# Kernel optimization log

Measured on AMD Instinct MI355X. Metric: run time of the kernel, lower is better.

The kernel has to match this reference:

```python
import jax, jax.numpy as jnp
import numpy as np

B, L, D, H, K = 2, 2048, 1024, 16, 32  # batch, seqlen, model dim, heads, max_rel_pos
DK = D // H


def setup_inputs() -> dict:
    key = jax.random.key(0)
    ks = jax.random.split(key, 12)
    inp = {
        "query": jax.random.normal(ks[0], (B, L, D), jnp.float32),
        "key": jax.random.normal(ks[1], (B, L, D), jnp.float32),
        "value": jax.random.normal(ks[2], (B, L, D), jnp.float32),
        "mask": jnp.ones((B, L, L), jnp.bool_),
        # Linear params (stored [in, out], applied x @ W + b)
        "Wq": jax.random.normal(ks[3], (D, D), jnp.float32) * 0.02,
        "bq": jnp.zeros((D,), jnp.float32),
        "Wk": jax.random.normal(ks[4], (D, D), jnp.float32) * 0.02,
        "bk": jnp.zeros((D,), jnp.float32),
        "Wv": jax.random.normal(ks[5], (D, D), jnp.float32) * 0.02,
        "bv": jnp.zeros((D,), jnp.float32),
        "Wo": jax.random.normal(ks[6], (D, D), jnp.float32) * 0.02,
        "bo": jnp.zeros((D,), jnp.float32),
        "rel_emb": jax.random.normal(ks[7], (2 * K + 1, DK), jnp.float32) * 0.02,
    }
    return inp


def _rel_pos_matrix(length, max_rel):
    r = jnp.arange(length)
    dist = r[None, :] - r[:, None]  # [i,j] = j - i
    return jnp.clip(dist, -max_rel, max_rel) + max_rel  # in [0, 2K]


def reference(query, key, value, mask, Wq, bq, Wk, bk, Wv, bv, Wo, bo, rel_emb):
    b, l, d = query.shape
    dk = d // H
    shape = lambda x: x.reshape(b, l, H, dk).transpose(0, 2, 1, 3)  # -> [b,h,l,dk]

    q = shape(query @ Wq + bq) / jnp.sqrt(jnp.asarray(dk, query.dtype))
    k = shape(key @ Wk + bk)
    v = shape(value @ Wv + bv)

    relpos = rel_emb[_rel_pos_matrix(l, K)]  # [l, l, dk]

    # scores: content + relative-key term
    scores = jnp.einsum("bhid,bhjd->bhij", q, k) + jnp.einsum("bhid,ijd->bhij", q, relpos)
    scores = jnp.where(mask[:, None, :, :], scores, -1e18)
    attn = jax.nn.softmax(scores, axis=-1)  # dropout is identity in eval

    # context: content + relative-value term
    ctx = jnp.einsum("bhij,bhjd->bhid", attn, v) + jnp.einsum("bhij,ijd->bhid", attn, relpos)
    x = ctx.transpose(0, 2, 1, 3).reshape(b, l, d)
    return x @ Wo + bo
```

## Files before the change

kernel.cpp:

```cpp
#include <hip/hip_runtime.h>
#include <hip/hip_bf16.h>
#include <stdint.h>

#define B_  2
#define L_  2048
#define D_  1024
#define H_  16
#define DK_ 64
#define M0L 6.0f
#define QSCALE 0.18033688011112042f
#define KVS 80

using bf16x8 = __attribute__((ext_vector_type(8))) short;
using f32x4  = __attribute__((ext_vector_type(4))) float;

static __device__ __forceinline__ unsigned short f2bf(float f) {
  unsigned int u = __builtin_bit_cast(unsigned int, f);
  u += 0x7FFFu + ((u >> 16) & 1u);
  return (unsigned short)(u >> 16);
}
static __device__ __forceinline__ float bf2f(unsigned short h) {
  unsigned int u = ((unsigned int)h) << 16;
  return __builtin_bit_cast(float, u);
}
static __device__ __forceinline__ unsigned packbf(float lo, float hi) {
  __hip_bfloat162 h2 = __float22bfloat162_rn(make_float2(lo, hi));
  unsigned r;
  __builtin_memcpy(&r, &h2, 4);
  return r;
}
static __device__ __forceinline__ bf16x8 mkfrag(unsigned a, unsigned b, unsigned c, unsigned d) {
  union { unsigned u[4]; bf16x8 v; } x;
  x.u[0] = a; x.u[1] = b; x.u[2] = c; x.u[3] = d;
  return x.v;
}
static __device__ __forceinline__ float aexp2(float x) {
  float r;
  asm("v_exp_f32 %0, %1" : "=v"(r) : "v"(x));
  return r;
}

__global__ __launch_bounds__(256) void k_prep(const float* __restrict__ q,
                                              const float* __restrict__ k,
                                              const float* __restrict__ v,
                                              unsigned short* __restrict__ xq,
                                              unsigned short* __restrict__ xk,
                                              unsigned short* __restrict__ xv,
                                              const float* __restrict__ W0,
                                              const float* __restrict__ W1,
                                              const float* __restrict__ W2,
                                              const float* __restrict__ W3,
                                              unsigned short* __restrict__ T0,
                                              unsigned short* __restrict__ T1,
                                              unsigned short* __restrict__ T2,
                                              unsigned short* __restrict__ T3) {
  __shared__ float ts[64][65];
  const int bx = blockIdx.x;
  const int tid = threadIdx.x;
  if (bx < 6144) {
    const int z = bx >> 11;
    const float* src = (z == 0) ? q : (z == 1) ? k : v;
    unsigned short* dst = (z == 0) ? xq : (z == 1) ? xk : xv;
    int i = (bx & 2047) * 256 + tid;
    float4 a = *(const float4*)(src + (size_t)i * 8);
    float4 b = *(const float4*)(src + (size_t)i * 8 + 4);
    union { unsigned short u[8]; uint4 v4; } o;
    o.u[0] = f2bf(a.x); o.u[1] = f2bf(a.y); o.u[2] = f2bf(a.z); o.u[3] = f2bf(a.w);
    o.u[4] = f2bf(b.x); o.u[5] = f2bf(b.y); o.u[6] = f2bf(b.z); o.u[7] = f2bf(b.w);
    *(uint4*)(dst + (size_t)i * 8) = o.v4;
  } else {
    const int r = bx - 6144;
    const int z = r >> 8, rem = r & 255;
    const float* W = (z == 0) ? W0 : (z == 1) ? W1 : (z == 2) ? W2 : W3;
    unsigned short* Wt = (z == 0) ? T0 : (z == 1) ? T1 : (z == 2) ? T2 : T3;
    const int n0 = (rem & 15) * 64, k0 = (rem >> 4) * 64;
#pragma unroll
    for (int it = 0; it < 4; ++it) {
      int idx = tid + it * 256;
      int row = idx >> 4, c4 = idx & 15;
      float4 vv = *(const float4*)&W[(size_t)(k0 + row) * 1024 + n0 + c4 * 4];
      ts[row][c4 * 4 + 0] = vv.x; ts[row][c4 * 4 + 1] = vv.y;
      ts[row][c4 * 4 + 2] = vv.z; ts[row][c4 * 4 + 3] = vv.w;
    }
    __syncthreads();
#pragma unroll
    for (int it = 0; it < 4; ++it) {
      int idx = tid + it * 256;
      int n = idx >> 4, c4 = idx & 15;
      ushort4 o;
      o.x = f2bf(ts[c4 * 4 + 0][n]); o.y = f2bf(ts[c4 * 4 + 1][n]);
      o.z = f2bf(ts[c4 * 4 + 2][n]); o.w = f2bf(ts[c4 * 4 + 3][n]);
      *(ushort4*)&Wt[(size_t)(n0 + n) * 1024 + k0 + c4 * 4] = o;
    }
  }
}

__global__ __launch_bounds__(256) void k_gemm_qkv(const unsigned short* __restrict__ XQ,
                                                  const unsigned short* __restrict__ XK,
                                                  const unsigned short* __restrict__ XV,
                                                  const unsigned short* __restrict__ WQ,
                                                  const unsigned short* __restrict__ WK,
                                                  const unsigned short* __restrict__ WV,
                                                  const float* __restrict__ bqp,
                                                  const float* __restrict__ bkp,
                                                  const float* __restrict__ bvp,
                                                  unsigned short* __restrict__ QBH,
                                                  unsigned short* __restrict__ KBH,
                                                  unsigned short* __restrict__ VT) {
  __shared__ __align__(16) unsigned short As[128 * 32];
  __shared__ __align__(16) unsigned short Bs[128 * 32];
  const int bid = blockIdx.x;
  const int xcd = bid & 7, nn = (bid >> 3) & 7, gq = bid >> 6;
  const int grp = gq * 8 + xcd;
  const int sel = grp >> 5, y = grp & 31;
  const unsigned short* X  = (sel == 0) ? XQ : (sel == 1) ? XK : XV;
  const unsigned short* Bt = (sel == 0) ? WQ : (sel == 1) ? WK : WV;
  const float* bias = (sel == 0) ? bqp : (sel == 1) ? bkp : bvp;
  const int tid = threadIdx.x;
  const int w = tid >> 6, lane = tid & 63;
  const int rl = lane & 15, kg = lane >> 4;
  const int wr = w >> 1, wc = w & 1;
  const int m0 = y * 128, n0 = nn * 128;
  const int arow = lane >> 2, acol = (lane & 3) * 8;

  const f32x4 fz = {0.f, 0.f, 0.f, 0.f};
  f32x4 acc[4][4];
#pragma unroll
  for (int m = 0; m < 4; ++m)
#pragma unroll
    for (int n = 0; n < 4; ++n) acc[m][n] = fz;

  for (int kt = 0; kt < 32; ++kt) {
    const int k0 = kt * 32;
    __syncthreads();
#pragma unroll
    for (int p = 0; p < 2; ++p) {
      int rowA = p * 64 + w * 16 + arow;
      const unsigned short* srcA = X + (size_t)(m0 + rowA) * 1024 + k0 + acol;
      __builtin_amdgcn_global_load_lds(
          (const __attribute__((address_space(1))) unsigned int*)srcA,
          (__attribute__((address_space(3))) unsigned int*)&As[(p * 64 + w * 16) * 32],
          16, 0, 0);
      const unsigned short* srcB = Bt + (size_t)(n0 + rowA) * 1024 + k0 + acol;
      __builtin_amdgcn_global_load_lds(
          (const __attribute__((address_space(1))) unsigned int*)srcB,
          (__attribute__((address_space(3))) unsigned int*)&Bs[(p * 64 + w * 16) * 32],
          16, 0, 0);
    }
    __syncthreads();
    bf16x8 aF[4], bF[4];
#pragma unroll
    for (int m = 0; m < 4; ++m)
      aF[m] = *reinterpret_cast<const bf16x8*>(&As[(wr * 64 + m * 16 + rl) * 32 + kg * 8]);
#pragma unroll
    for (int n = 0; n < 4; ++n)
      bF[n] = *reinterpret_cast<const bf16x8*>(&Bs[(wc * 64 + n * 16 + rl) * 32 + kg * 8]);
#pragma unroll
    for (int m = 0; m < 4; ++m)
#pragma unroll
      for (int n = 0; n < 4; ++n)
        acc[m][n] = __builtin_amdgcn_mfma_f32_16x16x32_bf16(aF[m], bF[n], acc[m][n], 0, 0, 0);
  }

  const float scale = (sel == 0) ? QSCALE : 1.0f;
  unsigned short* dstQK = (sel == 0) ? QBH : KBH;
#pragma unroll
  for (int m = 0; m < 4; ++m) {
#pragma unroll
    for (int n = 0; n < 4; ++n) {
      int ng = n0 + wc * 64 + n * 16 + rl;
      float bn = bias[ng];
      if (sel < 2) {
#pragma unroll
        for (int j = 0; j < 4; ++j) {
          int mg = m0 + wr * 64 + m * 16 + kg * 4 + j;
          float yv = (acc[m][n][j] + bn) * scale;
          int bb = mg >> 11, li = mg & 2047, hh = ng >> 6, dd = ng & 63;
          dstQK[(((size_t)(bb * H_ + hh)) * L_ + li) * DK_ + dd] = f2bf(yv);
        }
      } else {
        int mg0 = m0 + wr * 64 + m * 16 + kg * 4;
        int bb = mg0 >> 11, li = mg0 & 2047, hh = ng >> 6, dd = ng & 63;
        ushort4 o;
        o.x = f2bf(acc[m][n][0] + bn); o.y = f2bf(acc[m][n][1] + bn);
        o.z = f2bf(acc[m][n][2] + bn); o.w = f2bf(acc[m][n][3] + bn);
        *(ushort4*)&VT[((size_t)((bb * H_ + hh) * DK_ + dd)) * L_ + li] = o;
      }
    }
  }
}

__global__ __launch_bounds__(256) void k_gemm_out(const unsigned short* __restrict__ A,
                                                  const unsigned short* __restrict__ Bt,
                                                  const float* __restrict__ bias,
                                                  float* __restrict__ out) {
  __shared__ __align__(16) unsigned short As[128 * 32];
  __shared__ __align__(16) unsigned short Bs[64 * 32];
  const int bid = blockIdx.x;
  const int xcd = bid & 7, xn = (bid >> 3) & 15, yq = bid >> 7;
  const int y = yq * 8 + xcd;
  const int tid = threadIdx.x;
  const int w = tid >> 6, lane = tid & 63;
  const int rl = lane & 15, kg = lane >> 4;
  const int wr = w >> 1, wc = w & 1;
  const int m0 = y * 128, n0 = xn * 64;
  const int arow = lane >> 2, acol = (lane & 3) * 8;

  const f32x4 fz = {0.f, 0.f, 0.f, 0.f};
  f32x4 acc[4][2];
#pragma unroll
  for (int m = 0; m < 4; ++m)
#pragma unroll
    for (int n = 0; n < 2; ++n) acc[m][n] = fz;

  for (int kt = 0; kt < 32; ++kt) {
    const int k0 = kt * 32;
    __syncthreads();
#pragma unroll
    for (int p = 0; p < 2; ++p) {
      int row = w * 32 + p * 16 + arow;
      const unsigned short* src = A + (size_t)(m0 + row) * 1024 + k0 + acol;
      __builtin_amdgcn_global_load_lds(
          (const __attribute__((address_space(1))) unsigned int*)src,
          (__attribute__((address_space(3))) unsigned int*)&As[(w * 32 + p * 16) * 32],
          16, 0, 0);
    }
    {
      int row = w * 16 + arow;
      const unsigned short* src = Bt + (size_t)(n0 + row) * 1024 + k0 + acol;
      __builtin_amdgcn_global_load_lds(
          (const __attribute__((address_space(1))) unsigned int*)src,
          (__attribute__((address_space(3))) unsigned int*)&Bs[(w * 16) * 32],
          16, 0, 0);
    }
    __syncthreads();
    bf16x8 aF[4], bF[2];
#pragma unroll
    for (int m = 0; m < 4; ++m)
      aF[m] = *reinterpret_cast<const bf16x8*>(&As[(wr * 64 + m * 16 + rl) * 32 + kg * 8]);
#pragma unroll
    for (int n = 0; n < 2; ++n)
      bF[n] = *reinterpret_cast<const bf16x8*>(&Bs[(wc * 32 + n * 16 + rl) * 32 + kg * 8]);
#pragma unroll
    for (int m = 0; m < 4; ++m)
#pragma unroll
      for (int n = 0; n < 2; ++n)
        acc[m][n] = __builtin_amdgcn_mfma_f32_16x16x32_bf16(aF[m], bF[n], acc[m][n], 0, 0, 0);
  }

#pragma unroll
  for (int m = 0; m < 4; ++m) {
#pragma unroll
    for (int n = 0; n < 2; ++n) {
      int ng = n0 + wc * 32 + n * 16 + rl;
      float bn = bias[ng];
#pragma unroll
      for (int j = 0; j < 4; ++j) {
        int mg = m0 + wr * 64 + m * 16 + kg * 4 + j;
        out[(size_t)mg * 1024 + ng] = acc[m][n][j] + bn;
      }
    }
  }
}

struct KVT { unsigned short k[64 * KVS]; unsigned short v[64 * KVS]; };
union KVU {
  KVT t[2];
  unsigned short relx[9288];
};

__global__ __launch_bounds__(512, 4) void k_attn(const unsigned short* __restrict__ Qg,
                                                 const unsigned short* __restrict__ Kg,
                                                 const unsigned short* __restrict__ Vtg,
                                                 const float* __restrict__ rel,
                                                 unsigned short* __restrict__ ctxg) {
  __shared__ __align__(16) KVU kv;
  union SB {
    unsigned short q[128 * 72];
    struct {
      unsigned short qrel[128 * 65];
      unsigned short smid[128 * 72];
    } s;
  };
  __shared__ __align__(16) SB sb;

  const int tid = threadIdx.x;
  const int w = tid >> 6, lane = tid & 63;
  const int rl = lane & 15, kg = lane >> 4;
  const int i0 = blockIdx.x * 128;
  const int bh = blockIdx.y;
  const int bb = bh >> 4, hh = bh & 15;
  const int iw = i0 + w * 16;
  const int lrow = w * 16 + rl;
  const f32x4 fz = {0.f, 0.f, 0.f, 0.f};

  const int srow = tid >> 3, sc8 = tid & 7;
  auto load_kv = [&](int t, uint4& ko, uint4& vo) {
    ko = *(const uint4*)&Kg[((size_t)bh * L_ + t * 64 + srow) * DK_ + sc8 * 8];
    vo = *(const uint4*)&Vtg[((size_t)bh * DK_ + srow) * L_ + t * 64 + sc8 * 8];
  };
  auto stage_kv = [&](KVT& buf, const uint4& ko, const uint4& vo) {
    *(uint4*)&buf.k[srow * KVS + sc8 * 8] = ko;
    int hk = sc8 >> 2, tt = (sc8 >> 1) & 1;
    int kb1 = (2 * sc8) & 3, kb2 = (2 * sc8 + 1) & 3;
    *(uint2*)&buf.v[srow * KVS + hk * 32 + kb1 * 8 + tt * 4] = make_uint2(vo.x, vo.y);
    *(uint2*)&buf.v[srow * KVS + hk * 32 + kb2 * 8 + tt * 4] = make_uint2(vo.z, vo.w);
  };

  uint4 kA, vA, kB, vB;
  load_kv(0, kA, vA);
  load_kv(1, kB, vB);

#pragma unroll
  for (int it = 0; it < 2; ++it) {
    int s = tid + it * 512;
    int row = s >> 3, c8 = s & 7;
    uint4 v = *(const uint4*)&Qg[((size_t)bh * L_ + i0 + row) * DK_ + c8 * 8];
    *(uint4*)&sb.q[row * 72 + c8 * 8] = v;
  }
  for (int e = tid; e < 65 * 64; e += 512) {
    int r = e >> 6, d = e & 63;
    kv.relx[r * 72 + d] = f2bf(rel[e]);
  }
  __syncthreads();

  bf16x8 qB[2];
  qB[0] = *(const bf16x8*)&sb.q[lrow * 72 + kg * 8];
  qB[1] = *(const bf16x8*)&sb.q[lrow * 72 + 32 + kg * 8];
  __syncthreads();

#pragma unroll
  for (int rf = 0; rf < 5; ++rf) {
    int rrow = rf * 16 + rl; if (rrow > 64) rrow = 64;
    bf16x8 rA0 = *(const bf16x8*)&kv.relx[rrow * 72 + kg * 8];
    bf16x8 rA1 = *(const bf16x8*)&kv.relx[rrow * 72 + 32 + kg * 8];
    f32x4 qr = __builtin_amdgcn_mfma_f32_16x16x32_bf16(rA0, qB[0], fz, 0, 0, 0);
    qr = __builtin_amdgcn_mfma_f32_16x16x32_bf16(rA1, qB[1], qr, 0, 0, 0);
#pragma unroll
    for (int reg = 0; reg < 4; ++reg) {
      int r = rf * 16 + kg * 4 + reg;
      if (r <= 64) sb.s.qrel[lrow * 65 + r] = f2bf(qr[reg]);
    }
  }
  {
    unsigned* sm32 = (unsigned*)sb.s.smid;
    int base = w * 16 * 36;
    for (int e = lane; e < 16 * 36; e += 64) sm32[base + e] = 0xFF80FF80u;
  }

  float bL = bf2f(sb.s.qrel[lrow * 65 + 0]) - M0L;
  float bR = bf2f(sb.s.qrel[lrow * 65 + 64]) - M0L;

  f32x4 ctx[4];
#pragma unroll
  for (int df = 0; df < 4; ++df) ctx[df] = fz;
  float pL = 0.f, pR = 0.f, pM = 0.f;

  auto compute_tile = [&](const KVT& buf, int j0) {
    float pf[16];
    const int dclass = j0 - iw;
    if (dclass >= 48 || dclass <= -96) {
      const int isR = (dclass >= 48);
      const float bias = isR ? bR : bL;
      float ps = 0.f;
      __builtin_amdgcn_s_setprio(1);
#pragma unroll
      for (int kf = 0; kf < 4; ++kf) {
        bf16x8 kA0 = *(const bf16x8*)&buf.k[(kf * 16 + rl) * KVS + kg * 8];
        bf16x8 kA1 = *(const bf16x8*)&buf.k[(kf * 16 + rl) * KVS + 32 + kg * 8];
        f32x4 sa = __builtin_amdgcn_mfma_f32_16x16x32_bf16(kA0, qB[0], fz, 0, 0, 0);
        sa = __builtin_amdgcn_mfma_f32_16x16x32_bf16(kA1, qB[1], sa, 0, 0, 0);
#pragma unroll
        for (int reg = 0; reg < 4; ++reg) {
          float p = aexp2(sa[reg] + bias);
          ps += p;
          pf[kf * 4 + reg] = p;
        }
      }
      __builtin_amdgcn_s_setprio(0);
      if (isR) pR += ps; else pL += ps;
    } else {
#pragma unroll
      for (int kf = 0; kf < 4; ++kf) {
        bf16x8 kA0 = *(const bf16x8*)&buf.k[(kf * 16 + rl) * KVS + kg * 8];
        bf16x8 kA1 = *(const bf16x8*)&buf.k[(kf * 16 + rl) * KVS + 32 + kg * 8];
        f32x4 sa = __builtin_amdgcn_mfma_f32_16x16x32_bf16(kA0, qB[0], fz, 0, 0, 0);
        sa = __builtin_amdgcn_mfma_f32_16x16x32_bf16(kA1, qB[1], sa, 0, 0, 0);
#pragma unroll
        for (int reg = 0; reg < 4; ++reg) {
          int jj = kf * 16 + kg * 4 + reg;
          int dist = (j0 + jj) - (iw + rl);
          float p;
          if (dist <= -32) {
            p = aexp2(sa[reg] + bL);
            pL += p;
          } else if (dist >= 32) {
            p = aexp2(sa[reg] + bR);
            pR += p;
          } else {
            float qv = bf2f(sb.s.qrel[lrow * 65 + dist + 32]) - M0L;
            float sc = sa[reg] + qv;
            p = aexp2(sc);
            pM += p;
            sb.s.smid[lrow * 72 + dist + 32] = f2bf(sc);
          }
          pf[kf * 4 + reg] = p;
        }
      }
    }

    bf16x8 aP[2];
#pragma unroll
    for (int hk = 0; hk < 2; ++hk)
      aP[hk] = mkfrag(packbf(pf[8 * hk + 0], pf[8 * hk + 1]),
                      packbf(pf[8 * hk + 2], pf[8 * hk + 3]),
                      packbf(pf[8 * hk + 4], pf[8 * hk + 5]),
                      packbf(pf[8 * hk + 6], pf[8 * hk + 7]));

    __builtin_amdgcn_s_setprio(1);
#pragma unroll
    for (int df = 0; df < 4; ++df) {
      bf16x8 vF0 = *(const bf16x8*)&buf.v[(df * 16 + rl) * KVS + kg * 8];
      bf16x8 vF1 = *(const bf16x8*)&buf.v[(df * 16 + rl) * KVS + 32 + kg * 8];
      ctx[df] = __builtin_amdgcn_mfma_f32_16x16x32_bf16(aP[0], vF0, ctx[df], 0, 0, 0);
      ctx[df] = __builtin_amdgcn_mfma_f32_16x16x32_bf16(aP[1], vF1, ctx[df], 0, 0, 0);
    }
    __builtin_amdgcn_s_setprio(0);
  };

  __syncthreads();
  stage_kv(kv.t[0], kA, vA);
  load_kv(2, kA, vA);
  __syncthreads();

  for (int t = 0; t < 32; t += 2) {
    stage_kv(kv.t[1], kB, vB);
    if (t + 3 < 32) load_kv(t + 3, kB, vB);
    compute_tile(kv.t[0], t * 64);
    __syncthreads();
    if (t + 2 < 32) stage_kv(kv.t[0], kA, vA);
    if (t + 4 < 32) load_kv(t + 4, kA, vA);
    compute_tile(kv.t[1], (t + 1) * 64);
    __syncthreads();
  }

  for (int e = tid; e < 65 * 64; e += 512) {
    int r = e >> 6, d = e & 63;
    unsigned short v = f2bf(rel[e]);
    kv.relx[r * 72 + d] = v;
    kv.relx[4680 + d * 72 + r] = v;
  }
  __syncthreads();

  pL += __shfl_xor(pL, 16, 64); pL += __shfl_xor(pL, 32, 64);
  pR += __shfl_xor(pR, 16, 64); pR += __shfl_xor(pR, 32, 64);
  pM += __shfl_xor(pM, 16, 64); pM += __shfl_xor(pM, 32, 64);
  float invl = 1.0f / (pL + pR + pM);

  bf16x8 aA2[2];
#pragma unroll
  for (int hk = 0; hk < 2; ++hk) {
    float a2[8];
#pragma unroll
    for (int e = 0; e < 8; ++e)
      a2[e] = aexp2(bf2f(sb.s.smid[lrow * 72 + 32 * hk + kg * 8 + e]));
    aA2[hk] = mkfrag(packbf(a2[0], a2[1]), packbf(a2[2], a2[3]),
                     packbf(a2[4], a2[5]), packbf(a2[6], a2[7]));
  }
#pragma unroll
  for (int df = 0; df < 4; ++df) {
    bf16x8 rT0 = *(const bf16x8*)&kv.relx[4680 + (df * 16 + rl) * 72 + kg * 8];
    bf16x8 rT1 = *(const bf16x8*)&kv.relx[4680 + (df * 16 + rl) * 72 + 32 + kg * 8];
    ctx[df] = __builtin_amdgcn_mfma_f32_16x16x32_bf16(aA2[0], rT0, ctx[df], 0, 0, 0);
    ctx[df] = __builtin_amdgcn_mfma_f32_16x16x32_bf16(aA2[1], rT1, ctx[df], 0, 0, 0);
  }

  float invc[4], pLc[4], pRc[4];
#pragma unroll
  for (int reg = 0; reg < 4; ++reg) {
    int src = kg * 4 + reg;
    invc[reg] = __shfl(invl, src, 64);
    pLc[reg] = __shfl(pL, src, 64);
    pRc[reg] = __shfl(pR, src, 64);
  }

#pragma unroll
  for (int df = 0; df < 4; ++df) {
    float r0 = bf2f(kv.relx[0 * 72 + df * 16 + rl]);
    float r64 = bf2f(kv.relx[64 * 72 + df * 16 + rl]);
#pragma unroll
    for (int reg = 0; reg < 4; ++reg) {
      float val = (ctx[df][reg] + pLc[reg] * r0 + pRc[reg] * r64) * invc[reg];
      int ig = i0 + w * 16 + kg * 4 + reg;
      ctxg[((size_t)bb * L_ + ig) * D_ + hh * 64 + df * 16 + rl] = f2bf(val);
    }
  }
}

extern "C" void kernel_launch(void* const* d_in, const int* in_sizes, int n_in,
                              void* d_out, int out_size, void* d_ws, size_t ws_size,
                              hipStream_t stream) {
  (void)in_sizes; (void)n_in; (void)out_size; (void)ws_size;
  const float* query = (const float*)d_in[0];
  const float* key   = (const float*)d_in[1];
  const float* value = (const float*)d_in[2];
  const float* Wq = (const float*)d_in[4];  const float* bq = (const float*)d_in[5];
  const float* Wk = (const float*)d_in[6];  const float* bk = (const float*)d_in[7];
  const float* Wv = (const float*)d_in[8];  const float* bv = (const float*)d_in[9];
  const float* Wo = (const float*)d_in[10]; const float* bo = (const float*)d_in[11];
  const float* rel = (const float*)d_in[12];

  char* ws = (char*)d_ws;
  unsigned short* XQ  = (unsigned short*)(ws + 0);
  unsigned short* XK  = (unsigned short*)(ws + 8388608);
  unsigned short* XV  = (unsigned short*)(ws + 16777216);
  unsigned short* WTQ = (unsigned short*)(ws + 25165824);
  unsigned short* WTK = (unsigned short*)(ws + 27262976);
  unsigned short* WTV = (unsigned short*)(ws + 29360128);
  unsigned short* WTO = (unsigned short*)(ws + 31457280);
  unsigned short* QBH = (unsigned short*)(ws + 33554432);
  unsigned short* KBH = (unsigned short*)(ws + 41943040);
  unsigned short* VT  = (unsigned short*)(ws + 50331648);
  unsigned short* CTX = (unsigned short*)(ws + 58720256);

  k_prep<<<7168, 256, 0, stream>>>(query, key, value, XQ, XK, XV,
                                   Wq, Wk, Wv, Wo, WTQ, WTK, WTV, WTO);
  k_gemm_qkv<<<768, 256, 0, stream>>>(XQ, XK, XV, WTQ, WTK, WTV,
                                      bq, bk, bv, QBH, KBH, VT);
  k_attn<<<dim3(16, 32), 512, 0, stream>>>(QBH, KBH, VT, rel, CTX);
  k_gemm_out<<<512, 256, 0, stream>>>(CTX, WTO, bo, (float*)d_out);
}
```

Before: 145.6 us.

## Give each attention wave two 16-row query blocks to reuse K/V fragments

The attention kernel now runs 256 threads per block, with each wave handling 32 query rows (two 16-row sub-blocks) instead of 16. Each K and V fragment read from LDS feeds two MFMA chains, which halves LDS fragment traffic per unit of compute. The K/V staging loops and the softmax bookkeeping are widened to match. The cost is roughly double the accumulator and probability registers per thread and fewer waves per block, which may lower occupancy and latency hiding. The launch bounds change from (512,4) to (256,2).

```diff
diff --git a/kernel.cpp b/kernel.cpp
--- a/kernel.cpp
+++ b/kernel.cpp
@@ -269,7 +269,7 @@
   unsigned short relx[9288];
 };
 
-__global__ __launch_bounds__(512, 4) void k_attn(const unsigned short* __restrict__ Qg,
+__global__ __launch_bounds__(256, 2) void k_attn(const unsigned short* __restrict__ Qg,
                                                  const unsigned short* __restrict__ Kg,
                                                  const unsigned short* __restrict__ Vtg,
                                                  const float* __restrict__ rel,
@@ -290,43 +290,50 @@
   const int i0 = blockIdx.x * 128;
   const int bh = blockIdx.y;
   const int bb = bh >> 4, hh = bh & 15;
-  const int iw = i0 + w * 16;
-  const int lrow = w * 16 + rl;
+  const int iw = i0 + w * 32;
   const f32x4 fz = {0.f, 0.f, 0.f, 0.f};
 
   const int srow = tid >> 3, sc8 = tid & 7;
-  auto load_kv = [&](int t, uint4& ko, uint4& vo) {
-    ko = *(const uint4*)&Kg[((size_t)bh * L_ + t * 64 + srow) * DK_ + sc8 * 8];
-    vo = *(const uint4*)&Vtg[((size_t)bh * DK_ + srow) * L_ + t * 64 + sc8 * 8];
+  auto load_kv = [&](int t, uint4* ko, uint4* vo) {
+    ko[0] = *(const uint4*)&Kg[((size_t)bh * L_ + t * 64 + srow) * DK_ + sc8 * 8];
+    ko[1] = *(const uint4*)&Kg[((size_t)bh * L_ + t * 64 + 32 + srow) * DK_ + sc8 * 8];
+    vo[0] = *(const uint4*)&Vtg[((size_t)bh * DK_ + srow) * L_ + t * 64 + sc8 * 8];
+    vo[1] = *(const uint4*)&Vtg[((size_t)bh * DK_ + 32 + srow) * L_ + t * 64 + sc8 * 8];
   };
-  auto stage_kv = [&](KVT& buf, const uint4& ko, const uint4& vo) {
-    *(uint4*)&buf.k[srow * KVS + sc8 * 8] = ko;
+  auto stage_kv = [&](KVT& buf, const uint4* ko, const uint4* vo) {
+    *(uint4*)&buf.k[srow * KVS + sc8 * 8] = ko[0];
+    *(uint4*)&buf.k[(srow + 32) * KVS + sc8 * 8] = ko[1];
     int hk = sc8 >> 2, tt = (sc8 >> 1) & 1;
     int kb1 = (2 * sc8) & 3, kb2 = (2 * sc8 + 1) & 3;
-    *(uint2*)&buf.v[srow * KVS + hk * 32 + kb1 * 8 + tt * 4] = make_uint2(vo.x, vo.y);
-    *(uint2*)&buf.v[srow * KVS + hk * 32 + kb2 * 8 + tt * 4] = make_uint2(vo.z, vo.w);
+    *(uint2*)&buf.v[srow * KVS + hk * 32 + kb1 * 8 + tt * 4] = make_uint2(vo[0].x, vo[0].y);
+    *(uint2*)&buf.v[srow * KVS + hk * 32 + kb2 * 8 + tt * 4] = make_uint2(vo[0].z, vo[0].w);
+    *(uint2*)&buf.v[(srow + 32) * KVS + hk * 32 + kb1 * 8 + tt * 4] = make_uint2(vo[1].x, vo[1].y);
+    *(uint2*)&buf.v[(srow + 32) * KVS + hk * 32 + kb2 * 8 + tt * 4] = make_uint2(vo[1].z, vo[1].w);
   };
 
-  uint4 kA, vA, kB, vB;
+  uint4 kA[2], vA[2], kB[2], vB[2];
   load_kv(0, kA, vA);
   load_kv(1, kB, vB);
 
 #pragma unroll
-  for (int it = 0; it < 2; ++it) {
-    int s = tid + it * 512;
+  for (int it = 0; it < 4; ++it) {
+    int s = tid + it * 256;
     int row = s >> 3, c8 = s & 7;
     uint4 v = *(const uint4*)&Qg[((size_t)bh * L_ + i0 + row) * DK_ + c8 * 8];
     *(uint4*)&sb.q[row * 72 + c8 * 8] = v;
   }
-  for (int e = tid; e < 65 * 64; e += 512) {
+  for (int e = tid; e < 65 * 64; e += 256) {
     int r = e >> 6, d = e & 63;
     kv.relx[r * 72 + d] = f2bf(rel[e]);
   }
   __syncthreads();
 
-  bf16x8 qB[2];
-  qB[0] = *(const bf16x8*)&sb.q[lrow * 72 + kg * 8];
-  qB[1] = *(const bf16x8*)&sb.q[lrow * 72 + 32 + kg * 8];
+  bf16x8 qB[2][2];
+#pragma unroll
+  for (int ib = 0; ib < 2; ++ib) {
+    qB[ib][0] = *(const bf16x8*)&sb.q[(w * 32 + ib * 16 + rl) * 72 + kg * 8];
+    qB[ib][1] = *(const bf16x8*)&sb.q[(w * 32 + ib * 16 + rl) * 72 + 32 + kg * 8];
+  }
   __syncthreads();
 
 #pragma unroll
@@ -334,101 +341,113 @@
     int rrow = rf * 16 + rl; if (rrow > 64) rrow = 64;
     bf16x8 rA0 = *(const bf16x8*)&kv.relx[rrow * 72 + kg * 8];
     bf16x8 rA1 = *(const bf16x8*)&kv.relx[rrow * 72 + 32 + kg * 8];
-    f32x4 qr = __builtin_amdgcn_mfma_f32_16x16x32_bf16(rA0, qB[0], fz, 0, 0, 0);
-    qr = __builtin_amdgcn_mfma_f32_16x16x32_bf16(rA1, qB[1], qr, 0, 0, 0);
-#pragma unroll
-    for (int reg = 0; reg < 4; ++reg) {
-      int r = rf * 16 + kg * 4 + reg;
-      if (r <= 64) sb.s.qrel[lrow * 65 + r] = f2bf(qr[reg]);
+#pragma unroll
+    for (int ib = 0; ib < 2; ++ib) {
+      f32x4 qr = __builtin_amdgcn_mfma_f32_16x16x32_bf16(rA0, qB[ib][0], fz, 0, 0, 0);
+      qr = __builtin_amdgcn_mfma_f32_16x16x32_bf16(rA1, qB[ib][1], qr, 0, 0, 0);
+#pragma unroll
+      for (int reg = 0; reg < 4; ++reg) {
+        int r = rf * 16 + kg * 4 + reg;
+        if (r <= 64) sb.s.qrel[(w * 32 + ib * 16 + rl) * 65 + r] = f2bf(qr[reg]);
+      }
     }
   }
   {
     unsigned* sm32 = (unsigned*)sb.s.smid;
-    int base = w * 16 * 36;
-    for (int e = lane; e < 16 * 36; e += 64) sm32[base + e] = 0xFF80FF80u;
-  }
-
-  float bL = bf2f(sb.s.qrel[lrow * 65 + 0]) - M0L;
-  float bR = bf2f(sb.s.qrel[lrow * 65 + 64]) - M0L;
-
-  f32x4 ctx[4];
-#pragma unroll
-  for (int df = 0; df < 4; ++df) ctx[df] = fz;
-  float pL = 0.f, pR = 0.f, pM = 0.f;
+    for (int e = tid; e < 128 * 36; e += 256) sm32[e] = 0xFF80FF80u;
+  }
+  __syncthreads();
+
+  float bL[2], bR[2];
+#pragma unroll
+  for (int ib = 0; ib < 2; ++ib) {
+    int rowb = (w * 32 + ib * 16 + rl) * 65;
+    bL[ib] = bf2f(sb.s.qrel[rowb + 0]) - M0L;
+    bR[ib] = bf2f(sb.s.qrel[rowb + 64]) - M0L;
+  }
+
+  f32x4 ctx[2][4];
+#pragma unroll
+  for (int ib = 0; ib < 2; ++ib)
+#pragma unroll
+    for (int df = 0; df < 4; ++df) ctx[ib][df] = fz;
+  float pL[2] = {0.f, 0.f}, pR[2] = {0.f, 0.f}, pM[2] = {0.f, 0.f};
 
   auto compute_tile = [&](const KVT& buf, int j0) {
-    float pf[16];
+    float pf[2][16];
     const int dclass = j0 - iw;
-    if (dclass >= 48 || dclass <= -96) {
-      const int isR = (dclass >= 48);
-      const float bias = isR ? bR : bL;
-      float ps = 0.f;
-      __builtin_amdgcn_s_setprio(1);
-#pragma unroll
-      for (int kf = 0; kf < 4; ++kf) {
-        bf16x8 kA0 = *(const bf16x8*)&buf.k[(kf * 16 + rl) * KVS + kg * 8];
-        bf16x8 kA1 = *(const bf16x8*)&buf.k[(kf * 16 + rl) * KVS + 32 + kg * 8];
-        f32x4 sa = __builtin_amdgcn_mfma_f32_16x16x32_bf16(kA0, qB[0], fz, 0, 0, 0);
-        sa = __builtin_amdgcn_mfma_f32_16x16x32_bf16(kA1, qB[1], sa, 0, 0, 0);
-#pragma unroll
-        for (int reg = 0; reg < 4; ++reg) {
-          float p = aexp2(sa[reg] + bias);
-          ps += p;
-          pf[kf * 4 + reg] = p;
+#pragma unroll
+    for (int kf = 0; kf < 4; ++kf) {
+      bf16x8 kA0 = *(const bf16x8*)&buf.k[(kf * 16 + rl) * KVS + kg * 8];
+      bf16x8 kA1 = *(const bf16x8*)&buf.k[(kf * 16 + rl) * KVS + 32 + kg * 8];
+#pragma unroll
+      for (int ib = 0; ib < 2; ++ib) {
+        __builtin_amdgcn_s_setprio(1);
+        f32x4 sa = __builtin_amdgcn_mfma_f32_16x16x32_bf16(kA0, qB[ib][0], fz, 0, 0, 0);
+        sa = __builtin_amdgcn_mfma_f32_16x16x32_bf16(kA1, qB[ib][1], sa, 0, 0, 0);
+        __builtin_amdgcn_s_setprio(0);
+        const int dci = dclass - ib * 16;
+        if (dci >= 48 || dci <= -96) {
+          const int isR = (dci >= 48);
+          const float bias = isR ? bR[ib] : bL[ib];
+          float ps = 0.f;
+#pragma unroll
+          for (int reg = 0; reg < 4; ++reg) {
+            float p = aexp2(sa[reg] + bias);
+            ps += p;
+            pf[ib][kf * 4 + reg] = p;
+          }
+          if (isR) pR[ib] += ps; else pL[ib] += ps;
+        } else {
+          const int lrow = w * 32 + ib * 16 + rl;
+#pragma unroll
+          for (int reg = 0; reg < 4; ++reg) {
+            int jj = kf * 16 + kg * 4 + reg;
+            int dist = dci + jj - rl;
+            float p;
+            if (dist <= -32) {
+              p = aexp2(sa[reg] + bL[ib]);
+              pL[ib] += p;
+            } else if (dist >= 32) {
+              p = aexp2(sa[reg] + bR[ib]);
+              pR[ib] += p;
+            } else {
+              float qv = bf2f(sb.s.qrel[lrow * 65 + dist + 32]) - M0L;
+              float sc = sa[reg] + qv;
+              p = aexp2(sc);
+              pM[ib] += p;
+              sb.s.smid[lrow * 72 + dist + 32] = f2bf(sc);
+            }
+            pf[ib][kf * 4 + reg] = p;
+          }
         }
       }
-      __builtin_amdgcn_s_setprio(0);
-      if (isR) pR += ps; else pL += ps;
-    } else {
-#pragma unroll
-      for (int kf = 0; kf < 4; ++kf) {
-        bf16x8 kA0 = *(const bf16x8*)&buf.k[(kf * 16 + rl) * KVS + kg * 8];
-        bf16x8 kA1 = *(const bf16x8*)&buf.k[(kf * 16 + rl) * KVS + 32 + kg * 8];
-        f32x4 sa = __builtin_amdgcn_mfma_f32_16x16x32_bf16(kA0, qB[0], fz, 0, 0, 0);
-        sa = __builtin_amdgcn_mfma_f32_16x16x32_bf16(kA1, qB[1], sa, 0, 0, 0);
-#pragma unroll
-        for (int reg = 0; reg < 4; ++reg) {
-          int jj = kf * 16 + kg * 4 + reg;
-          int dist = (j0 + jj) - (iw + rl);
-          float p;
-          if (dist <= -32) {
-            p = aexp2(sa[reg] + bL);
-            pL += p;
-          } else if (dist >= 32) {
-            p = aexp2(sa[reg] + bR);
-            pR += p;
-          } else {
-            float qv = bf2f(sb.s.qrel[lrow * 65 + dist + 32]) - M0L;
-            float sc = sa[reg] + qv;
-            p = aexp2(sc);
-            pM += p;
-            sb.s.smid[lrow * 72 + dist + 32] = f2bf(sc);
-          }
-          pf[kf * 4 + reg] = p;
-        }
-      }
-    }
-
-    bf16x8 aP[2];
-#pragma unroll
-    for (int hk = 0; hk < 2; ++hk)
-      aP[hk] = mkfrag(packbf(pf[8 * hk + 0], pf[8 * hk + 1]),
-                      packbf(pf[8 * hk + 2], pf[8 * hk + 3]),
-                      packbf(pf[8 * hk + 4], pf[8 * hk + 5]),
-                      packbf(pf[8 * hk + 6], pf[8 * hk + 7]));
+    }
+
+    bf16x8 aP[2][2];
+#pragma unroll
+    for (int ib = 0; ib < 2; ++ib)
+#pragma unroll
+      for (int hk = 0; hk < 2; ++hk)
+        aP[ib][hk] = mkfrag(packbf(pf[ib][8 * hk + 0], pf[ib][8 * hk + 1]),
+                            packbf(pf[ib][8 * hk + 2], pf[ib][8 * hk + 3]),
+                            packbf(pf[ib][8 * hk + 4], pf[ib][8 * hk + 5]),
+                            packbf(pf[ib][8 * hk + 6], pf[ib][8 * hk + 7]));
 
     __builtin_amdgcn_s_setprio(1);
 #pragma unroll
     for (int df = 0; df < 4; ++df) {
       bf16x8 vF0 = *(const bf16x8*)&buf.v[(df * 16 + rl) * KVS + kg * 8];
       bf16x8 vF1 = *(const bf16x8*)&buf.v[(df * 16 + rl) * KVS + 32 + kg * 8];
-      ctx[df] = __builtin_amdgcn_mfma_f32_16x16x32_bf16(aP[0], vF0, ctx[df], 0, 0, 0);
-      ctx[df] = __builtin_amdgcn_mfma_f32_16x16x32_bf16(aP[1], vF1, ctx[df], 0, 0, 0);
+#pragma unroll
+      for (int ib = 0; ib < 2; ++ib) {
+        ctx[ib][df] = __builtin_amdgcn_mfma_f32_16x16x32_bf16(aP[ib][0], vF0, ctx[ib][df], 0, 0, 0);
+        ctx[ib][df] = __builtin_amdgcn_mfma_f32_16x16x32_bf16(aP[ib][1], vF1, ctx[ib][df], 0, 0, 0);
+      }
     }
     __builtin_amdgcn_s_setprio(0);
   };
 
-  __syncthreads();
   stage_kv(kv.t[0], kA, vA);
   load_kv(2, kA, vA);
   __syncthreads();
@@ -444,56 +463,71 @@
     __syncthreads();
   }
 
-  for (int e = tid; e < 65 * 64; e += 512) {
+  for (int e = tid; e < 65 * 64; e += 256) {
     int r = e >> 6, d = e & 63;
     unsigned short v = f2bf(rel[e]);
     kv.relx[r * 72 + d] = v;
     kv.relx[4680 + d * 72 + r] = v;
   }
+#pragma unroll
+  for (int ib = 0; ib < 2; ++ib) {
+    pL[ib] += __shfl_xor(pL[ib], 16, 64); pL[ib] += __shfl_xor(pL[ib], 32, 64);
+    pR[ib] += __shfl_xor(pR[ib], 16, 64); pR[ib] += __shfl_xor(pR[ib], 32, 64);
+    pM[ib] += __shfl_xor(pM[ib], 16, 64); pM[ib] += __shfl_xor(pM[ib], 32, 64);
+  }
+  float invl[2];
+  invl[0] = 1.0f / (pL[0] + pR[0] + pM[0]);
+  invl[1] = 1.0f / (pL[1] + pR[1] + pM[1]);
   __syncthreads();
 
-  pL += __shfl_xor(pL, 16, 64); pL += __shfl_xor(pL, 32, 64);
-  pR += __shfl_xor(pR, 16, 64); pR += __shfl_xor(pR, 32, 64);
-  pM += __shfl_xor(pM, 16, 64); pM += __shfl_xor(pM, 32, 64);
-  float invl = 1.0f / (pL + pR + pM);
-
-  bf16x8 aA2[2];
-#pragma unroll
-  for (int hk = 0; hk < 2; ++hk) {
-    float a2[8];
-#pragma unroll
-    for (int e = 0; e < 8; ++e)
-      a2[e] = aexp2(bf2f(sb.s.smid[lrow * 72 + 32 * hk + kg * 8 + e]));
-    aA2[hk] = mkfrag(packbf(a2[0], a2[1]), packbf(a2[2], a2[3]),
-                     packbf(a2[4], a2[5]), packbf(a2[6], a2[7]));
+  bf16x8 aA2[2][2];
+#pragma unroll
+  for (int ib = 0; ib < 2; ++ib) {
+    const int lrow = w * 32 + ib * 16 + rl;
+#pragma unroll
+    for (int hk = 0; hk < 2; ++hk) {
+      float a2[8];
+#pragma unroll
+      for (int e = 0; e < 8; ++e)
+        a2[e] = aexp2(bf2f(sb.s.smid[lrow * 72 + 32 * hk + kg * 8 + e]));
+      aA2[ib][hk] = mkfrag(packbf(a2[0], a2[1]), packbf(a2[2], a2[3]),
+                           packbf(a2[4], a2[5]), packbf(a2[6], a2[7]));
+    }
   }
 #pragma unroll
   for (int df = 0; df < 4; ++df) {
     bf16x8 rT0 = *(const bf16x8*)&kv.relx[4680 + (df * 16 + rl) * 72 + kg * 8];
     bf16x8 rT1 = *(const bf16x8*)&kv.relx[4680 + (df * 16 + rl) * 72 + 32 + kg * 8];
-    ctx[df] = __builtin_amdgcn_mfma_f32_16x16x32_bf16(aA2[0], rT0, ctx[df], 0, 0, 0);
-    ctx[df] = __builtin_amdgcn_mfma_f32_16x16x32_bf16(aA2[1], rT1, ctx[df], 0, 0, 0);
-  }
-
-  float invc[4], pLc[4], pRc[4];
-#pragma unroll
-  for (int reg = 0; reg < 4; ++reg) {
-    int src = kg * 4 + reg;
-    invc[reg] = __shfl(invl, src, 64);
-    pLc[reg] = __shfl(pL, src, 64);
-    pRc[reg] = __shfl(pR, src, 64);
-  }
+#pragma unroll
+    for (int ib = 0; ib < 2; ++ib) {
+      ctx[ib][df] = __builtin_amdgcn_mfma_f32_16x16x32_bf16(aA2[ib][0], rT0, ctx[ib][df], 0, 0, 0);
+      ctx[ib][df] = __builtin_amdgcn_mfma_f32_16x16x32_bf16(aA2[ib][1], rT1, ctx[ib][df], 0, 0, 0);
+    }
+  }
+
+  float invc[2][4], pLc[2][4], pRc[2][4];
+#pragma unroll
+  for (int ib = 0; ib < 2; ++ib)
+#pragma unroll
+    for (int reg = 0; reg < 4; ++reg) {
+      int src = kg * 4 + reg;
+      invc[ib][reg] = __shfl(invl[ib], src, 64);
+      pLc[ib][reg] = __shfl(pL[ib], src, 64);
+      pRc[ib][reg] = __shfl(pR[ib], src, 64);
+    }
 
 #pragma unroll
   for (int df = 0; df < 4; ++df) {
     float r0 = bf2f(kv.relx[0 * 72 + df * 16 + rl]);
     float r64 = bf2f(kv.relx[64 * 72 + df * 16 + rl]);
 #pragma unroll
-    for (int reg = 0; reg < 4; ++reg) {
-      float val = (ctx[df][reg] + pLc[reg] * r0 + pRc[reg] * r64) * invc[reg];
-      int ig = i0 + w * 16 + kg * 4 + reg;
-      ctxg[((size_t)bb * L_ + ig) * D_ + hh * 64 + df * 16 + rl] = f2bf(val);
-    }
+    for (int ib = 0; ib < 2; ++ib)
+#pragma unroll
+      for (int reg = 0; reg < 4; ++reg) {
+        float val = (ctx[ib][df][reg] + pLc[ib][reg] * r0 + pRc[ib][reg] * r64) * invc[ib][reg];
+        int ig = i0 + w * 32 + ib * 16 + kg * 4 + reg;
+        ctxg[((size_t)bb * L_ + ig) * D_ + hh * 64 + df * 16 + rl] = f2bf(val);
+      }
   }
 }
 
@@ -527,6 +561,6 @@
                                    Wq, Wk, Wv, Wo, WTQ, WTK, WTV, WTO);
   k_gemm_qkv<<<768, 256, 0, stream>>>(XQ, XK, XV, WTQ, WTK, WTV,
                                       bq, bk, bv, QBH, KBH, VT);
-  k_attn<<<dim3(16, 32), 512, 0, stream>>>(QBH, KBH, VT, rel, CTX);
+  k_attn<<<dim3(16, 32), 256, 0, stream>>>(QBH, KBH, VT, rel, CTX);
   k_gemm_out<<<512, 256, 0, stream>>>(CTX, WTO, bo, (float*)d_out);
 }
```

Result: slower. 175.3 us (+20.4%).
